# Kernel optimization log

Measured on AMD Instinct MI355X. Metric: run time of the kernel, lower is better.

The kernel has to match this reference:

```python
import jax, jax.numpy as jnp
import numpy as np

B, IN, H, K = 4096, 1024, 1024, 32  # batch, input_size, hidden_size, inner_hidden


def setup_inputs() -> dict:
    key = jax.random.key(0)
    ks = jax.random.split(key, 11)
    stdv = 1.0 / np.sqrt(H)
    u = lambda k, shp: jax.random.uniform(k, shp, jnp.float32, -stdv, stdv)
    return {
        "x": jax.random.normal(ks[0], (B, IN), jnp.float32),
        "h_prev": jax.random.normal(ks[1], (B, H), jnp.float32),
        "c_prev": jax.random.normal(ks[2], (B, H), jnp.float32),
        "Wg": u(ks[3], (3 * H, IN + H)),
        "bg": u(ks[4], (3 * H,)),
        "Wc": u(ks[5], (2 * H, IN + H)),
        "bc": u(ks[6], (2 * H,)),
        "W1": u(ks[7], (K, 2)),
        "b1": u(ks[8], (K,)),
        "W2": u(ks[9], (1, K)),
        "b2": u(ks[10], (1,)),
    }


def reference(x, h_prev, c_prev, Wg, bg, Wc, bc, W1, b1, W2, b2):
    combined = jnp.concatenate([x, h_prev], axis=1)          # [B, IN+H]
    gates = combined @ Wg.T + bg                              # [B, 3H]
    i, f, o = jnp.split(jax.nn.sigmoid(gates), 3, axis=1)     # each [B, H]
    cell_raw = combined @ Wc.T + bc                           # [B, 2H]
    pairs = cell_raw.reshape(B, H, 2)                         # [B, H, 2]
    hid = jax.nn.relu(jnp.einsum('bhp,kp->bhk', pairs, W1) + b1)  # [B, H, K]
    g = jnp.einsum('bhk,ok->bho', hid, W2)[..., 0] + b2[0]    # [B, H]
    c_next = f * c_prev + i * g
    h_next = o * jnp.tanh(c_next)
    return (h_next, c_next)
```

## Files before the change

kernel.cpp:

```cpp
#include <hip/hip_runtime.h>
#include <hip/hip_bf16.h>

#define BB   4096
#define INW  1024
#define HH   1024
#define KIN  2048
#define NG   5120
#define KH   32
#define FPG  10
#define NTG  32

typedef __bf16 bf16;
typedef __bf16 bf16x4 __attribute__((ext_vector_type(4)));
typedef __bf16 bf16x8 __attribute__((ext_vector_type(8)));
typedef float  floatx4 __attribute__((ext_vector_type(4)));

#define GLD16(gp, lp)                                                          \
  __builtin_amdgcn_global_load_lds(                                            \
      (__attribute__((address_space(1))) const void*)(gp),                     \
      (__attribute__((address_space(3))) void*)(lp), 16, 0, 0)

#define NCB  4096
#define NWB  1280

__global__ __launch_bounds__(256) void prep(
    const float* __restrict__ x, const float* __restrict__ h,
    const float* __restrict__ Wg, const float* __restrict__ Wc,
    bf16* __restrict__ comb, bf16* __restrict__ Wb) {
  int tid = threadIdx.x;
  if (blockIdx.x < NCB) {
    int e = (blockIdx.x * 256 + tid) * 8;
    int b = e >> 11;
    int c = e & (KIN - 1);
    const float* src = (c < INW) ? (x + (size_t)b * INW + c)
                                 : (h + (size_t)b * HH + (c - INW));
    float4 v0 = *(const float4*)src;
    float4 v1 = *(const float4*)(src + 4);
    bf16x8 ov;
    ov[0] = (bf16)v0.x; ov[1] = (bf16)v0.y; ov[2] = (bf16)v0.z; ov[3] = (bf16)v0.w;
    ov[4] = (bf16)v1.x; ov[5] = (bf16)v1.y; ov[6] = (bf16)v1.z; ov[7] = (bf16)v1.w;
    *(bf16x8*)(comb + e) = ov;
  } else {
    int w   = blockIdx.x - NCB;
    int nt  = w / 40;
    int rem = w - nt * 40;
    int f   = rem >> 2;
    int rp  = rem & 3;
    int q   = f / 5;
    int g   = f - q * 5;
    int kk  = tid >> 2;
    int kq  = tid & 3;
    size_t wbase = ((size_t)(nt * FPG + f) * 64 + kk) * 64 + kq * 16;
#pragma unroll
    for (int r4 = 0; r4 < 4; ++r4) {
      int s    = rp * 4 + r4;
      int hcol = nt * 32 + q * 16 + s;
      const float* src = (g < 3)
          ? (Wg + (size_t)(g * HH + hcol) * KIN + tid * 8)
          : (Wc + (size_t)(2 * hcol + (g - 3)) * KIN + tid * 8);
      float4 v0 = *(const float4*)src;
      float4 v1 = *(const float4*)(src + 4);
      bf16x8 ov;
      ov[0] = (bf16)v0.x; ov[1] = (bf16)v0.y; ov[2] = (bf16)v0.z; ov[3] = (bf16)v0.w;
      ov[4] = (bf16)v1.x; ov[5] = (bf16)v1.y; ov[6] = (bf16)v1.z; ov[7] = (bf16)v1.w;
      *(bf16x8*)(Wb + (wbase + s) * 8) = ov;
    }
  }
}

#define ASZ  8192
#define BSZ  10240
#define BUF  (ASZ + BSZ)

__global__ __launch_bounds__(512, 4) void gemm_fused(
    const bf16* __restrict__ A, const bf16* __restrict__ Bm,
    const float* __restrict__ c_prev, const float* __restrict__ bg,
    const float* __restrict__ bc, const float* __restrict__ W1,
    const float* __restrict__ b1, const float* __restrict__ W2,
    const float* __restrict__ b2, float* __restrict__ h_next,
    float* __restrict__ c_next) {
  __shared__ bf16 sh[2 * BUF];

  const int tid  = threadIdx.x;
  const int wave = tid >> 6;
  const int lane = tid & 63;

  const int bid = blockIdx.y * gridDim.x + blockIdx.x;
  const int swz = (bid & 7) * 128 + (bid >> 3);
  const int m0  = (swz & 31) * 128;
  const int nt  = swz >> 5;

  const int wm = (wave >> 1) * 32;
  const int q  = wave & 1;
  const int lr = lane & 15;
  const int qd = lane >> 4;

  floatx4 acc[2][5] = {};

#define STAGE(bb, kt)                                                          \
  {                                                                            \
    if (wave < 4) {                                                            \
      _Pragma("unroll")                                                        \
      for (int j = 0; j < 4; ++j) {                                            \
        int s   = j * 256 + tid;                                               \
        int row = s >> 3;                                                      \
        int c   = (s & 7) ^ (row & 7);                                         \
        GLD16(A + (size_t)(m0 + row) * KIN + (kt) * 64 + c * 8,                \
              sh + (size_t)(bb) * BUF + (size_t)(j * 256 + wave * 64) * 8);    \
      }                                                                        \
    } else {                                                                   \
      int wv = wave - 4;                                                       \
      _Pragma("unroll")                                                        \
      for (int j = 0; j < 5; ++j) {                                            \
        int s   = j * 256 + wv * 64 + lane;                                    \
        int c20 = s >> 6;                                                      \
        int f   = c20 >> 1;                                                    \
        int ks  = c20 & 1;                                                     \
        size_t gchunk = (size_t)(nt * FPG + f) * 64 + ((kt) * 2 + ks);         \
        GLD16(Bm + (gchunk * 64 + lane) * 8,                                   \
              sh + (size_t)(bb) * BUF + ASZ + (size_t)s * 8);                  \
      }                                                                        \
    }                                                                          \
  }

#define COMPUTE(bb)                                                            \
  {                                                                            \
    const bf16* As = sh + (size_t)(bb) * BUF;                                  \
    const bf16* Bs = As + ASZ;                                                 \
    _Pragma("unroll")                                                          \
    for (int ks = 0; ks < 2; ++ks) {                                           \
      bf16x8 af[2];                                                            \
      _Pragma("unroll")                                                        \
      for (int mi = 0; mi < 2; ++mi) {                                         \
        int row  = wm + mi * 16 + lr;                                          \
        int slot = (ks * 4 + qd) ^ (lr & 7);                                   \
        af[mi] = *(const bf16x8*)&As[(row << 6) + (slot << 3)];                \
      }                                                                        \
      bf16x8 bfr[5];                                                           \
      _Pragma("unroll")                                                        \
      for (int ni = 0; ni < 5; ++ni) {                                         \
        int chunk = ((q * 5 + ni) << 1) + ks;                                  \
        bfr[ni] = *(const bf16x8*)&Bs[(chunk << 9) + (lane << 3)];             \
      }                                                                        \
      _Pragma("unroll")                                                        \
      for (int mi = 0; mi < 2; ++mi)                                           \
        _Pragma("unroll")                                                      \
        for (int ni = 0; ni < 5; ++ni)                                         \
          acc[mi][ni] = __builtin_amdgcn_mfma_f32_16x16x32_bf16(               \
              af[mi], bfr[ni], acc[mi][ni], 0, 0, 0);                          \
    }                                                                          \
  }

  STAGE(0, 0);
  __syncthreads();

  for (int kt = 0; kt < KIN / 64 - 1; ++kt) {
    const int cur = kt & 1;
    STAGE(cur ^ 1, kt + 1);
    COMPUTE(cur);
    __syncthreads();
  }
  COMPUTE(1);

  const int h   = nt * 32 + q * 16 + lr;
  const float bgi = bg[h];
  const float bgf = bg[HH + h];
  const float bgo = bg[2 * HH + h];
  const float bc0 = bc[2 * h];
  const float bc1 = bc[2 * h + 1];
  const float gb  = b2[0];

  float p0[8], p1[8], ga[8];
#pragma unroll
  for (int mi = 0; mi < 2; ++mi)
#pragma unroll
    for (int r = 0; r < 4; ++r) {
      p0[mi * 4 + r] = acc[mi][3][r] + bc0;
      p1[mi * 4 + r] = acc[mi][4][r] + bc1;
      ga[mi * 4 + r] = gb;
    }
#pragma unroll
  for (int k = 0; k < KH; ++k) {
    float w0 = W1[2 * k], w1 = W1[2 * k + 1], bk = b1[k], wk = W2[k];
#pragma unroll
    for (int e = 0; e < 8; ++e) {
      float hv = fmaf(p0[e], w0, fmaf(p1[e], w1, bk));
      hv = fmaxf(hv, 0.0f);
      ga[e] = fmaf(hv, wk, ga[e]);
    }
  }

#pragma unroll
  for (int mi = 0; mi < 2; ++mi)
#pragma unroll
    for (int r = 0; r < 4; ++r) {
      int b    = m0 + wm + mi * 16 + qd * 4 + r;
      size_t o = (size_t)b * HH + h;
      float si = 1.0f / (1.0f + __expf(-(acc[mi][0][r] + bgi)));
      float sf = 1.0f / (1.0f + __expf(-(acc[mi][1][r] + bgf)));
      float so = 1.0f / (1.0f + __expf(-(acc[mi][2][r] + bgo)));
      float cn = fmaf(sf, c_prev[o], si * ga[mi * 4 + r]);
      float e2 = __expf(2.0f * cn);
      float th = 1.0f - 2.0f / (e2 + 1.0f);
      h_next[o] = so * th;
      c_next[o] = cn;
    }
}

extern "C" void kernel_launch(void* const* d_in, const int* in_sizes, int n_in,
                              void* d_out, int out_size, void* d_ws, size_t ws_size,
                              hipStream_t stream) {
  const float* x      = (const float*)d_in[0];
  const float* h_prev = (const float*)d_in[1];
  const float* c_prev = (const float*)d_in[2];
  const float* Wg     = (const float*)d_in[3];
  const float* bg     = (const float*)d_in[4];
  const float* Wc     = (const float*)d_in[5];
  const float* bc     = (const float*)d_in[6];
  const float* W1     = (const float*)d_in[7];
  const float* b1     = (const float*)d_in[8];
  const float* W2     = (const float*)d_in[9];
  const float* b2     = (const float*)d_in[10];
  float* out = (float*)d_out;

  char* ws = (char*)d_ws;
  bf16* comb = (bf16*)ws;
  bf16* Wb   = (bf16*)(ws + (size_t)BB * KIN * 2);

  prep<<<NCB + NWB, 256, 0, stream>>>(x, h_prev, Wg, Wc, comb, Wb);

  dim3 grid(BB / 128, NTG);
  gemm_fused<<<grid, 512, 0, stream>>>(comb, Wb, c_prev, bg, bc, W1, b1, W2,
                                       b2, out, out + (size_t)BB * HH);
}
```

Baseline: 243.3 us.

## Triple-buffer LDS pipeline with split staging, manual vmcnt waits and MFMA priority

Replaces the double-buffered LDS main loop with a three-buffer ring that prefetches two k-tiles ahead. Each k-tile's global-to-LDS loads are split across the two half-iterations and interleaved with fragment loads and MFMAs. Explicit s_waitcnt vmcnt and raw s_barrier calls (fenced by sched_barrier) replace __syncthreads, and s_setprio raises priority around the MFMA bursts. The goal is to hide global load latency and barrier stalls. The larger LDS footprint and the change of launch bounds from 4 to 2 may lower occupancy, and the hand-counted waits are fragile.

After: 267.4 us. 9.9% more time.

```diff
diff --git a/kernel.cpp b/kernel.cpp
--- a/kernel.cpp
+++ b/kernel.cpp
@@ -72,14 +72,14 @@
 #define BSZ  10240
 #define BUF  (ASZ + BSZ)
 
-__global__ __launch_bounds__(512, 4) void gemm_fused(
+__global__ __launch_bounds__(512, 2) void gemm_fused(
     const bf16* __restrict__ A, const bf16* __restrict__ Bm,
     const float* __restrict__ c_prev, const float* __restrict__ bg,
     const float* __restrict__ bc, const float* __restrict__ W1,
     const float* __restrict__ b1, const float* __restrict__ W2,
     const float* __restrict__ b2, float* __restrict__ h_next,
     float* __restrict__ c_next) {
-  __shared__ bf16 sh[2 * BUF];
+  __shared__ bf16 sh[3 * BUF];
 
   const int tid  = threadIdx.x;
   const int wave = tid >> 6;
@@ -97,70 +97,106 @@
 
   floatx4 acc[2][5] = {};
 
-#define STAGE(bb, kt)                                                          \
+#define STG(bb, kt, JA0, JA1, JB0, JB1)                                        \
   {                                                                            \
     if (wave < 4) {                                                            \
       _Pragma("unroll")                                                        \
-      for (int j = 0; j < 4; ++j) {                                            \
+      for (int j = (JA0); j <= (JA1); ++j) {                                   \
         int s   = j * 256 + tid;                                               \
         int row = s >> 3;                                                      \
         int c   = (s & 7) ^ (row & 7);                                         \
         GLD16(A + (size_t)(m0 + row) * KIN + (kt) * 64 + c * 8,                \
-              sh + (size_t)(bb) * BUF + (size_t)(j * 256 + wave * 64) * 8);    \
+              sh + (size_t)(bb) * BUF + (size_t)s * 8);                        \
       }                                                                        \
     } else {                                                                   \
       int wv = wave - 4;                                                       \
       _Pragma("unroll")                                                        \
-      for (int j = 0; j < 5; ++j) {                                            \
+      for (int j = (JB0); j <= (JB1); ++j) {                                   \
         int s   = j * 256 + wv * 64 + lane;                                    \
-        int c20 = s >> 6;                                                      \
+        int c20 = j * 4 + wv;                                                  \
         int f   = c20 >> 1;                                                    \
-        int ks  = c20 & 1;                                                     \
-        size_t gchunk = (size_t)(nt * FPG + f) * 64 + ((kt) * 2 + ks);         \
+        int ks2 = c20 & 1;                                                     \
+        size_t gchunk = (size_t)(nt * FPG + f) * 64 + ((kt) * 2 + ks2);        \
         GLD16(Bm + (gchunk * 64 + lane) * 8,                                   \
               sh + (size_t)(bb) * BUF + ASZ + (size_t)s * 8);                  \
       }                                                                        \
     }                                                                          \
   }
 
-#define COMPUTE(bb)                                                            \
-  {                                                                            \
-    const bf16* As = sh + (size_t)(bb) * BUF;                                  \
-    const bf16* Bs = As + ASZ;                                                 \
+#define LDFRAG(af, bf, ks)                                                     \
+  {                                                                            \
     _Pragma("unroll")                                                          \
-    for (int ks = 0; ks < 2; ++ks) {                                           \
-      bf16x8 af[2];                                                            \
+    for (int mi = 0; mi < 2; ++mi) {                                           \
+      int row  = wm + mi * 16 + lr;                                            \
+      int slot = ((ks) * 4 + qd) ^ (lr & 7);                                   \
+      af[mi] = *(const bf16x8*)&As[(row << 6) + (slot << 3)];                  \
+    }                                                                          \
+    _Pragma("unroll")                                                          \
+    for (int ni = 0; ni < 5; ++ni) {                                           \
+      int chunk = ((q * 5 + ni) << 1) + (ks);                                  \
+      bf[ni] = *(const bf16x8*)&Bs[(chunk << 9) + (lane << 3)];                \
+    }                                                                          \
+  }
+
+#define MFMA10(af, bf)                                                         \
+  {                                                                            \
+    _Pragma("unroll")                                                          \
+    for (int mi = 0; mi < 2; ++mi)                                             \
       _Pragma("unroll")                                                        \
-      for (int mi = 0; mi < 2; ++mi) {                                         \
-        int row  = wm + mi * 16 + lr;                                          \
-        int slot = (ks * 4 + qd) ^ (lr & 7);                                   \
-        af[mi] = *(const bf16x8*)&As[(row << 6) + (slot << 3)];                \
-      }                                                                        \
-      bf16x8 bfr[5];                                                           \
-      _Pragma("unroll")                                                        \
-      for (int ni = 0; ni < 5; ++ni) {                                         \
-        int chunk = ((q * 5 + ni) << 1) + ks;                                  \
-        bfr[ni] = *(const bf16x8*)&Bs[(chunk << 9) + (lane << 3)];             \
-      }                                                                        \
-      _Pragma("unroll")                                                        \
-      for (int mi = 0; mi < 2; ++mi)                                           \
-        _Pragma("unroll")                                                      \
-        for (int ni = 0; ni < 5; ++ni)                                         \
-          acc[mi][ni] = __builtin_amdgcn_mfma_f32_16x16x32_bf16(               \
-              af[mi], bfr[ni], acc[mi][ni], 0, 0, 0);                          \
-    }                                                                          \
-  }
-
-  STAGE(0, 0);
-  __syncthreads();
-
-  for (int kt = 0; kt < KIN / 64 - 1; ++kt) {
-    const int cur = kt & 1;
-    STAGE(cur ^ 1, kt + 1);
-    COMPUTE(cur);
-    __syncthreads();
-  }
-  COMPUTE(1);
+      for (int ni = 0; ni < 5; ++ni)                                           \
+        acc[mi][ni] = __builtin_amdgcn_mfma_f32_16x16x32_bf16(                 \
+            af[mi], bf[ni], acc[mi][ni], 0, 0, 0);                             \
+  }
+
+#define VMW()                                                                  \
+  {                                                                            \
+    if (wave < 4) asm volatile("s_waitcnt vmcnt(4)" ::: "memory");             \
+    else          asm volatile("s_waitcnt vmcnt(5)" ::: "memory");             \
+  }
+
+#define BAR()                                                                  \
+  {                                                                            \
+    __builtin_amdgcn_sched_barrier(0);                                         \
+    __builtin_amdgcn_s_barrier();                                              \
+    __builtin_amdgcn_sched_barrier(0);                                         \
+  }
+
+  STG(0, 0, 0, 3, 0, 4);
+  STG(1, 1, 0, 3, 0, 4);
+  VMW();
+  BAR();
+
+  int u = 0, v = 2;
+#pragma unroll 1
+  for (int t = 0; t < 32; ++t) {
+    const bf16* As = sh + (size_t)u * BUF;
+    const bf16* Bs = As + ASZ;
+    const int ts = (t + 2 < 32) ? t + 2 : 31;
+    {
+      bf16x8 af0[2], bf0[5];
+      LDFRAG(af0, bf0, 0);
+      STG(v, ts, 0, 1, 0, 1);
+      BAR();
+      __builtin_amdgcn_s_setprio(1);
+      MFMA10(af0, bf0);
+      __builtin_amdgcn_s_setprio(0);
+      __builtin_amdgcn_sched_barrier(0);
+    }
+    {
+      bf16x8 af1[2], bf1[5];
+      LDFRAG(af1, bf1, 1);
+      STG(v, ts, 2, 3, 2, 4);
+      VMW();
+      BAR();
+      __builtin_amdgcn_s_setprio(1);
+      MFMA10(af1, bf1);
+      __builtin_amdgcn_s_setprio(0);
+      __builtin_amdgcn_sched_barrier(0);
+    }
+    u = (u == 2) ? 0 : u + 1;
+    v = (v == 2) ? 0 : v + 1;
+  }
+  asm volatile("s_waitcnt vmcnt(0)" ::: "memory");
 
   const int h   = nt * 32 + q * 16 + lr;
   const float bgi = bg[h];
```
